# Kernel optimization log

Hardware: AMD Instinct MI355X
Metric: run time of the kernel (lower is better)

Reference implementation:

```python
import jax, jax.numpy as jnp
import numpy as np

HIDDEN = 2048
INTER = 768
NUM_EXPERTS = 32
TOP_K = 4
NUM_TOKENS = 2048


def setup_inputs() -> dict:
    key = jax.random.key(0)
    ks = jax.random.split(key, 5)
    scale = 0.02
    x = jax.random.normal(ks[0], (NUM_TOKENS, HIDDEN), dtype=jnp.float32)
    w_router = jax.random.normal(ks[1], (HIDDEN, NUM_EXPERTS), dtype=jnp.float32) * scale
    w_gate = jax.random.normal(ks[2], (NUM_EXPERTS, HIDDEN, INTER), dtype=jnp.float32) * scale
    w_up = jax.random.normal(ks[3], (NUM_EXPERTS, HIDDEN, INTER), dtype=jnp.float32) * scale
    w_down = jax.random.normal(ks[4], (NUM_EXPERTS, INTER, HIDDEN), dtype=jnp.float32) * scale
    return {"hidden_states": x, "w_router": w_router, "w_gate": w_gate,
            "w_up": w_up, "w_down": w_down}


def reference(hidden_states, w_router, w_gate, w_up, w_down):
    x = hidden_states  # [T, H]
    T = x.shape[0]
    # Router: softmax over experts (in input dtype), top-k, renormalize.
    router_logits = x @ w_router                      # [T, E]
    routing_weights = jax.nn.softmax(router_logits, axis=-1)
    top_w, top_idx = jax.lax.top_k(routing_weights, TOP_K)  # [T, K]
    top_w = top_w / jnp.sum(top_w, axis=-1, keepdims=True)   # norm_topk_prob
    # Dense combine weights: combine[t, e] = routing weight if expert e selected
    # for token t, else 0.  (top-k indices are unique per token.)
    combine = jnp.zeros((T, NUM_EXPERTS), dtype=x.dtype)
    combine = combine.at[jnp.arange(T)[:, None], top_idx].add(top_w)  # [T, E]

    # Scan over experts: each step computes one expert's SwiGLU MLP on all
    # tokens and accumulates it weighted by its combine weight (tokens with
    # zero weight contribute nothing, matching the gather/scatter original).
    def body(acc, expert):
        wg, wu, wd, cw = expert  # [H,I], [H,I], [I,H], [T]
        h = jax.nn.silu(x @ wg) * (x @ wu)   # [T, I]
        return acc + (h @ wd) * cw[:, None], None

    out, _ = jax.lax.scan(body, jnp.zeros_like(x),
                          (w_gate, w_up, w_down, combine.T))
    return out
```

## Files before the change

### kernel.cpp

```cpp
#include <hip/hip_runtime.h>

#define T_TOK 2048
#define HID   2048
#define INTER 768
#define NE    32
#define NSLOT 8192
#define MAXT  96

typedef short bf16x8 __attribute__((ext_vector_type(8)));
typedef float f32x4  __attribute__((ext_vector_type(4)));

#if defined(__has_builtin)
#  if __has_builtin(__builtin_amdgcn_global_load_lds)
#    define HAS_GLDS 1
#  endif
#endif
#ifndef HAS_GLDS
#  define HAS_GLDS 0
#endif

__device__ __forceinline__ unsigned short f2b(float f){
  unsigned u = __builtin_bit_cast(unsigned, f);
  u += 0x7fffu + ((u >> 16) & 1u);
  return (unsigned short)(u >> 16);
}
__device__ __forceinline__ unsigned pk2(float a, float b){
  return (unsigned)f2b(a) | ((unsigned)f2b(b) << 16);
}

__device__ __forceinline__ void stageA16(const ushort* gsrc, ushort* ldst){
#if HAS_GLDS
  __builtin_amdgcn_global_load_lds(
      (const __attribute__((address_space(1))) unsigned int*)gsrc,
      (__attribute__((address_space(3))) unsigned int*)ldst, 16, 0, 0);
#else
  *(uint4*)ldst = *(const uint4*)gsrc;
#endif
}

#define XB_OFF    0ul
#define HBUF_OFF  8388608ul
#define TKW_OFF   20971520ul
#define TKI_OFF   21004288ul
#define ROWS_OFF  21037056ul
#define WTS_OFF   21069824ul
#define OFFS_OFF  21102592ul
#define LOGIT_OFF 21102848ul
#define CNT_OFF   21364992ul
#define FILL_OFF  21365120ul
#define TLIST_OFF 21365248ul
#define T2S_OFF   21365760ul
#define HB2_OFF   21398528ul
#define WS_NEED   (HB2_OFF + 67108864ul)
#define ZERO_OFF  21102848ul
#define ZERO_SZ   (262144ul + 128ul + 128ul)

__global__ void convert_x_kernel(const float* __restrict__ x, ushort* __restrict__ xb){
  int i = (blockIdx.x * 256 + threadIdx.x) * 8;
  float4 a = *(const float4*)(x + i);
  float4 b = *(const float4*)(x + i + 4);
  uint4 o;
  o.x = pk2(a.x, a.y);
  o.y = pk2(a.z, a.w);
  o.z = pk2(b.x, b.y);
  o.w = pk2(b.z, b.w);
  *(uint4*)(xb + i) = o;
}

__global__ void router_gemm(const float* __restrict__ x, const float* __restrict__ wr,
                            float* __restrict__ logits){
  const int tt = blockIdx.x;
  const int kb = blockIdx.y;
  __shared__ float xs[64 * 64];
  __shared__ float wsm[64 * 32];
  const int tid = threadIdx.x;
  const int r = tid >> 5, e = tid & 31;
  float acc[8];
#pragma unroll
  for (int i = 0; i < 8; i++) acc[i] = 0.0f;

  for (int sub = 0; sub < 4; ++sub){
    const int k0 = kb * 256 + sub * 64;
    __syncthreads();
#pragma unroll
    for (int j = 0; j < 4; j++){
      int f4 = tid + j * 256;
      int row = f4 >> 4, c4 = f4 & 15;
      float4 v = *(const float4*)(x + (size_t)(tt * 64 + row) * HID + k0 + c4 * 4);
      *(float4*)(xs + row * 64 + c4 * 4) = v;
    }
#pragma unroll
    for (int j = 0; j < 2; j++){
      int f4 = tid + j * 256;
      int row = f4 >> 3, c4 = f4 & 7;
      float4 v = *(const float4*)(wr + (size_t)(k0 + row) * NE + c4 * 4);
      *(float4*)(wsm + row * NE + c4 * 4) = v;
    }
    __syncthreads();
    for (int kk = 0; kk < 64; kk++){
      float wv = wsm[kk * NE + e];
#pragma unroll
      for (int i = 0; i < 8; i++) acc[i] += xs[(r + i * 8) * 64 + kk] * wv;
    }
  }
#pragma unroll
  for (int i = 0; i < 8; i++)
    atomicAdd(&logits[(size_t)(tt * 64 + r + i * 8) * NE + e], acc[i]);
}

__global__ void topk_kernel(const float* __restrict__ logits, float* __restrict__ topk_w,
                            int* __restrict__ topk_i, int* __restrict__ counts){
  int t = blockIdx.x * blockDim.x + threadIdx.x;
  if (t >= T_TOK) return;
  float l[32];
  const float4* lp = (const float4*)(logits + (size_t)t * NE);
#pragma unroll
  for (int i = 0; i < 8; i++){
    float4 v = lp[i];
    l[i*4+0] = v.x; l[i*4+1] = v.y; l[i*4+2] = v.z; l[i*4+3] = v.w;
  }
  float m = l[0];
#pragma unroll
  for (int i = 1; i < 32; i++) m = fmaxf(m, l[i]);
#pragma unroll
  for (int i = 0; i < 32; i++) l[i] = __expf(l[i] - m);
  float wsel[4]; int isel[4];
#pragma unroll
  for (int k = 0; k < 4; k++){
    float best = l[0]; int bi = 0;
#pragma unroll
    for (int i = 1; i < 32; i++){ if (l[i] > best){ best = l[i]; bi = i; } }
    wsel[k] = best; isel[k] = bi; l[bi] = -1.0f;
  }
  float s4 = wsel[0] + wsel[1] + wsel[2] + wsel[3];
  float inv = 1.0f / s4;
#pragma unroll
  for (int k = 0; k < 4; k++){
    topk_w[t * 4 + k] = wsel[k] * inv;
    topk_i[t * 4 + k] = isel[k];
    atomicAdd(&counts[isel[k]], 1);
  }
}

__global__ void prefix_kernel(const int* __restrict__ counts, int* __restrict__ offsets,
                              int* __restrict__ tlist){
  if (threadIdx.x == 0){
    int a = 0; offsets[0] = 0; int nt_ = 0;
    for (int e = 0; e < NE; e++){
      int c = counts[e];
      for (int m = 0; m * 128 < c && nt_ < MAXT; m++) tlist[nt_++] = e | (m << 16);
      a += c; offsets[e + 1] = a;
    }
    for (; nt_ < MAXT; nt_++) tlist[nt_] = -1;
  }
}

__global__ void scatter_kernel(const int* __restrict__ topk_i, const float* __restrict__ topk_w,
                               const int* __restrict__ offsets, int* __restrict__ fill,
                               int* __restrict__ rows, float* __restrict__ wts,
                               int* __restrict__ t2s){
  int gid = blockIdx.x * 256 + threadIdx.x;
  int t = gid >> 2;
  int e = topk_i[gid];
  int pos = atomicAdd(&fill[e], 1);
  int s = offsets[e] + pos;
  rows[s] = t;
  wts[s] = topk_w[gid];
  t2s[gid] = s;
}

#define NT_GU 64
#define GU_BUF 8192
__global__ __launch_bounds__(512, 6) void gateup_kernel(
    const ushort* __restrict__ xb, const float* __restrict__ wg,
    const float* __restrict__ wu, const int* __restrict__ rows,
    const float* __restrict__ wts, const int* __restrict__ counts,
    const int* __restrict__ offsets, const int* __restrict__ tlist,
    ushort* __restrict__ hbuf)
{
  const int w = tlist[blockIdx.y];
  if (w < 0) return;
  const int e = w & 0xffff, mt = w >> 16;
  const int nt = blockIdx.x;
  const int cnt = counts[e];
  const int off = offsets[e];
  const int n0 = nt * 64;

  __shared__ __align__(16) ushort lds[2 * GU_BUF];

  const int tid = threadIdx.x;

  const int ar = tid >> 2, adc = tid & 3;
  const int alc = adc ^ ((ar >> 1) & 3);
  const int srow = mt * 128 + ar;
  const int tokA = rows[off + (srow < cnt ? srow : 0)];
  const ushort* agp = xb + (size_t)tokA * HID + alc * 8;

  const int bn = tid & 63, kg = tid >> 6;
  const size_t wofs = (size_t)e * (HID * INTER) + (size_t)(kg * 4) * INTER + n0 + bn;
  const float* wgp = wg + wofs;
  const float* wup = wu + wofs;
  const int bofs = bn * 32 + ((kg >> 1) ^ ((bn >> 1) & 3)) * 8 + (kg & 1) * 4;

  const int lane = tid & 63, wv = tid >> 6;
  const int wm = wv >> 1, wn = wv & 1;
  const int fr = lane & 15, ko = lane >> 4;

  int aoff[2], boff[2];
#pragma unroll
  for (int mf = 0; mf < 2; mf++){
    int r = wm * 32 + mf * 16 + fr;
    aoff[mf] = r * 32 + ((ko ^ ((r >> 1) & 3)) * 8);
  }
#pragma unroll
  for (int nf = 0; nf < 2; nf++){
    int c = wn * 32 + nf * 16 + fr;
    boff[nf] = c * 32 + ((ko ^ ((c >> 1) & 3)) * 8);
  }

  f32x4 accg[2][2], accu[2][2];
#pragma unroll
  for (int i = 0; i < 2; i++)
#pragma unroll
    for (int j = 0; j < 2; j++){ accg[i][j] = (f32x4)(0.0f); accu[i][j] = (f32x4)(0.0f); }

  float sg[4], su[4];

  auto loadB = [&](int k0){
    const float* pg_ = wgp + (size_t)k0 * INTER;
    const float* pu_ = wup + (size_t)k0 * INTER;
#pragma unroll
    for (int kk = 0; kk < 4; kk++){ sg[kk] = pg_[(size_t)kk * INTER]; su[kk] = pu_[(size_t)kk * INTER]; }
  };
  auto writeB = [&](int base){
    uint2 pg, pu;
    pg.x = pk2(sg[0], sg[1]); pg.y = pk2(sg[2], sg[3]);
    pu.x = pk2(su[0], su[1]); pu.y = pk2(su[2], su[3]);
    *(uint2*)(lds + base + 4096 + bofs) = pg;
    *(uint2*)(lds + base + 6144 + bofs) = pu;
  };
  auto computeTile = [&](int base){
    bf16x8 a[2], bg2[2], bu2[2];
#pragma unroll
    for (int mf = 0; mf < 2; mf++) a[mf] = *(const bf16x8*)(lds + base + aoff[mf]);
#pragma unroll
    for (int nf = 0; nf < 2; nf++){
      bg2[nf] = *(const bf16x8*)(lds + base + 4096 + boff[nf]);
      bu2[nf] = *(const bf16x8*)(lds + base + 6144 + boff[nf]);
    }
#pragma unroll
    for (int mf = 0; mf < 2; mf++)
#pragma unroll
      for (int nf = 0; nf < 2; nf++){
        accg[mf][nf] = __builtin_amdgcn_mfma_f32_16x16x32_bf16(a[mf], bg2[nf], accg[mf][nf], 0, 0, 0);
        accu[mf][nf] = __builtin_amdgcn_mfma_f32_16x16x32_bf16(a[mf], bu2[nf], accu[mf][nf], 0, 0, 0);
      }
  };

  stageA16(agp, lds + tid * 8);
  loadB(0);
  writeB(0);
  __syncthreads();

  int cb = 0;
  for (int t = 0; t < NT_GU; ++t){
    const int nb = cb ^ GU_BUF;
    if (t + 1 < NT_GU){
      stageA16(agp + (t + 1) * 32, lds + nb + tid * 8);
      loadB((t + 1) * 32);
    }
    computeTile(cb);
    if (t + 1 < NT_GU) writeB(nb);
    __syncthreads();
    cb = nb;
  }

#pragma unroll
  for (int mf = 0; mf < 2; mf++)
#pragma unroll
    for (int j = 0; j < 4; j++){
      int rl = wm * 32 + mf * 16 + ko * 4 + j;
      int gr = mt * 128 + rl;
      if (gr < cnt){
        float w2 = wts[off + gr];
        size_t robase = (size_t)(off + gr) * INTER + n0;
#pragma unroll
        for (int nf = 0; nf < 2; nf++){
          float g = accg[mf][nf][j], u = accu[mf][nf][j];
          float h = (g / (1.0f + __expf(-g))) * u * w2;
          hbuf[robase + wn * 32 + nf * 16 + fr] = f2b(h);
        }
      }
    }
}

#define NT_DN 24
#define DN_BUF 6144
template<bool SLOT>
__global__ __launch_bounds__(512, 6) void down_kernel(
    const ushort* __restrict__ hbuf, const float* __restrict__ wd,
    const int* __restrict__ rows, const int* __restrict__ counts,
    const int* __restrict__ offsets, const int* __restrict__ tlist,
    float* __restrict__ outp)
{
  const int w = tlist[blockIdx.y];
  if (w < 0) return;
  const int e = w & 0xffff, mt = w >> 16;
  const int nt = blockIdx.x;
  const int cnt = counts[e];
  const int off = offsets[e];
  const int n0 = nt * 64;

  __shared__ __align__(16) ushort lds[2 * DN_BUF];

  const int tid = threadIdx.x;

  const int ar = tid >> 2, adc = tid & 3;
  const int alc = adc ^ ((ar >> 1) & 3);
  const int srow = mt * 128 + ar;
  const int slotA = off + (srow < cnt ? srow : 0);
  const ushort* agp = hbuf + (size_t)slotA * INTER + alc * 8;

  const int bn = tid & 63, kg = tid >> 6;
  const float* wdp = wd + (size_t)e * (INTER * HID) + (size_t)(kg * 4) * HID + n0 + bn;
  const int bofs = bn * 32 + ((kg >> 1) ^ ((bn >> 1) & 3)) * 8 + (kg & 1) * 4;

  const int lane = tid & 63, wv = tid >> 6;
  const int wm = wv >> 1, wn = wv & 1;
  const int fr = lane & 15, ko = lane >> 4;

  int aoff[2], boff[2];
#pragma unroll
  for (int mf = 0; mf < 2; mf++){
    int r = wm * 32 + mf * 16 + fr;
    aoff[mf] = r * 32 + ((ko ^ ((r >> 1) & 3)) * 8);
  }
#pragma unroll
  for (int nf = 0; nf < 2; nf++){
    int c = wn * 32 + nf * 16 + fr;
    boff[nf] = c * 32 + ((ko ^ ((c >> 1) & 3)) * 8);
  }

  f32x4 acc[2][2];
#pragma unroll
  for (int i = 0; i < 2; i++)
#pragma unroll
    for (int j = 0; j < 2; j++) acc[i][j] = (f32x4)(0.0f);

  float sb[4];

  auto loadB = [&](int k0){
    const float* p = wdp + (size_t)k0 * HID;
#pragma unroll
    for (int kk = 0; kk < 4; kk++) sb[kk] = p[(size_t)kk * HID];
  };
  auto writeB = [&](int base){
    uint2 pb;
    pb.x = pk2(sb[0], sb[1]); pb.y = pk2(sb[2], sb[3]);
    *(uint2*)(lds + base + 4096 + bofs) = pb;
  };
  auto computeTile = [&](int base){
    bf16x8 a[2], b2[2];
#pragma unroll
    for (int mf = 0; mf < 2; mf++) a[mf] = *(const bf16x8*)(lds + base + aoff[mf]);
#pragma unroll
    for (int nf = 0; nf < 2; nf++) b2[nf] = *(const bf16x8*)(lds + base + 4096 + boff[nf]);
#pragma unroll
    for (int mf = 0; mf < 2; mf++)
#pragma unroll
      for (int nf = 0; nf < 2; nf++)
        acc[mf][nf] = __builtin_amdgcn_mfma_f32_16x16x32_bf16(a[mf], b2[nf], acc[mf][nf], 0, 0, 0);
  };

  stageA16(agp, lds + tid * 8);
  loadB(0);
  writeB(0);
  __syncthreads();

  int cb = 0;
  for (int t = 0; t < NT_DN; ++t){
    const int nb = cb ^ DN_BUF;
    if (t + 1 < NT_DN){
      stageA16(agp + (t + 1) * 32, lds + nb + tid * 8);
      loadB((t + 1) * 32);
    }
    computeTile(cb);
    if (t + 1 < NT_DN) writeB(nb);
    __syncthreads();
    cb = nb;
  }

#pragma unroll
  for (int mf = 0; mf < 2; mf++)
#pragma unroll
    for (int j = 0; j < 4; j++){
      int rl = wm * 32 + mf * 16 + ko * 4 + j;
      int gr = mt * 128 + rl;
      if (gr < cnt){
        if (SLOT){
          float* obase = outp + (size_t)(off + gr) * HID + n0;
#pragma unroll
          for (int nf = 0; nf < 2; nf++)
            obase[wn * 32 + nf * 16 + fr] = acc[mf][nf][j];
        } else {
          int tok = rows[off + gr];
          float* obase = outp + (size_t)tok * HID + n0;
#pragma unroll
          for (int nf = 0; nf < 2; nf++)
            atomicAdd(obase + wn * 32 + nf * 16 + fr, acc[mf][nf][j]);
        }
      }
    }
}

__global__ void combine_kernel(const float* __restrict__ hbuf2, const int* __restrict__ t2s,
                               float* __restrict__ out){
  const int t = blockIdx.y;
  const int c4 = (blockIdx.x * 256 + threadIdx.x) * 4;
  const int s0 = t2s[t * 4 + 0], s1 = t2s[t * 4 + 1];
  const int s2 = t2s[t * 4 + 2], s3 = t2s[t * 4 + 3];
  float4 a = *(const float4*)(hbuf2 + (size_t)s0 * HID + c4);
  float4 b = *(const float4*)(hbuf2 + (size_t)s1 * HID + c4);
  float4 c = *(const float4*)(hbuf2 + (size_t)s2 * HID + c4);
  float4 d = *(const float4*)(hbuf2 + (size_t)s3 * HID + c4);
  float4 r;
  r.x = a.x + b.x + c.x + d.x;
  r.y = a.y + b.y + c.y + d.y;
  r.z = a.z + b.z + c.z + d.z;
  r.w = a.w + b.w + c.w + d.w;
  *(float4*)(out + (size_t)t * HID + c4) = r;
}

extern "C" void kernel_launch(void* const* d_in, const int* in_sizes, int n_in,
                              void* d_out, int out_size, void* d_ws, size_t ws_size,
                              hipStream_t stream){
  const float* x  = (const float*)d_in[0];
  const float* wr = (const float*)d_in[1];
  const float* wg = (const float*)d_in[2];
  const float* wu = (const float*)d_in[3];
  const float* wd = (const float*)d_in[4];
  float* out = (float*)d_out;
  char* ws = (char*)d_ws;

  ushort* xb     = (ushort*)(ws + XB_OFF);
  ushort* hbuf   = (ushort*)(ws + HBUF_OFF);
  float*  topkw  = (float*)(ws + TKW_OFF);
  int*    topki  = (int*)(ws + TKI_OFF);
  int*    rows   = (int*)(ws + ROWS_OFF);
  float*  wts    = (float*)(ws + WTS_OFF);
  int*    offs   = (int*)(ws + OFFS_OFF);
  float*  logits = (float*)(ws + LOGIT_OFF);
  int*    counts = (int*)(ws + CNT_OFF);
  int*    fill   = (int*)(ws + FILL_OFF);
  int*    tlist  = (int*)(ws + TLIST_OFF);
  int*    t2s    = (int*)(ws + T2S_OFF);
  float*  hbuf2  = (float*)(ws + HB2_OFF);

  const bool slotpath = (ws_size >= WS_NEED);

  hipMemsetAsync(ws + ZERO_OFF, 0, ZERO_SZ, stream);

  convert_x_kernel<<<2048, 256, 0, stream>>>(x, xb);
  router_gemm<<<dim3(32, 8), 256, 0, stream>>>(x, wr, logits);
  topk_kernel<<<8, 256, 0, stream>>>(logits, topkw, topki, counts);
  prefix_kernel<<<1, 64, 0, stream>>>(counts, offs, tlist);
  scatter_kernel<<<32, 256, 0, stream>>>(topki, topkw, offs, fill, rows, wts, t2s);
  gateup_kernel<<<dim3(12, MAXT), 512, 0, stream>>>(xb, wg, wu, rows, wts, counts, offs, tlist, hbuf);
  if (slotpath){
    down_kernel<true><<<dim3(32, MAXT), 512, 0, stream>>>(hbuf, wd, rows, counts, offs, tlist, hbuf2);
    combine_kernel<<<dim3(2, T_TOK), 256, 0, stream>>>(hbuf2, t2s, out);
  } else {
    hipMemsetAsync(d_out, 0, (size_t)out_size * sizeof(float), stream);
    down_kernel<false><<<dim3(32, MAXT), 512, 0, stream>>>(hbuf, wd, rows, counts, offs, tlist, out);
  }
}
```

Before: 365.0 us.

## Enlarge MoE GEMM tiles, split gate/up into separate blocks, add SwiGLU fuse kernel

Gate/up and down GEMMs move from 128x64 to 128x256 output tiles, with 16 MFMA accumulators per wave and float4 weight loads in place of scalar strided loads. Gate and up projections now run in separate blocks that write bf16 intermediates. A new elementwise kernel applies SiLU, the multiply and the routing weight. The slot-buffer plus combine path is dropped, so the down projection always accumulates into the output with atomics. The aim is better weight-load coalescing and more operand reuse per tile. The cost is fewer blocks per grid, an extra intermediate round trip, and atomic contention on the output.

```diff
diff --git a/kernel.cpp b/kernel.cpp
--- a/kernel.cpp
+++ b/kernel.cpp
@@ -27,6 +27,10 @@
 __device__ __forceinline__ unsigned pk2(float a, float b){
   return (unsigned)f2b(a) | ((unsigned)f2b(b) << 16);
 }
+__device__ __forceinline__ float b2f(unsigned short u){
+  unsigned x = ((unsigned)u) << 16;
+  return __builtin_bit_cast(float, x);
+}
 
 __device__ __forceinline__ void stageA16(const ushort* gsrc, ushort* ldst){
 #if HAS_GLDS
@@ -39,7 +43,7 @@
 }
 
 #define XB_OFF    0ul
-#define HBUF_OFF  8388608ul
+#define GBUF_OFF  8388608ul
 #define TKW_OFF   20971520ul
 #define TKI_OFF   21004288ul
 #define ROWS_OFF  21037056ul
@@ -49,9 +53,7 @@
 #define CNT_OFF   21364992ul
 #define FILL_OFF  21365120ul
 #define TLIST_OFF 21365248ul
-#define T2S_OFF   21365760ul
-#define HB2_OFF   21398528ul
-#define WS_NEED   (HB2_OFF + 67108864ul)
+#define UBUF_OFF  21365760ul
 #define ZERO_OFF  21102848ul
 #define ZERO_SZ   (262144ul + 128ul + 128ul)
 
@@ -157,8 +159,7 @@
 
 __global__ void scatter_kernel(const int* __restrict__ topk_i, const float* __restrict__ topk_w,
                                const int* __restrict__ offsets, int* __restrict__ fill,
-                               int* __restrict__ rows, float* __restrict__ wts,
-                               int* __restrict__ t2s){
+                               int* __restrict__ rows, float* __restrict__ wts){
   int gid = blockIdx.x * 256 + threadIdx.x;
   int t = gid >> 2;
   int e = topk_i[gid];
@@ -166,95 +167,228 @@
   int s = offsets[e] + pos;
   rows[s] = t;
   wts[s] = topk_w[gid];
-  t2s[gid] = s;
 }
 
 #define NT_GU 64
-#define GU_BUF 8192
-__global__ __launch_bounds__(512, 6) void gateup_kernel(
+#define LDS_STRIDE 12288
+__global__ __launch_bounds__(512) void guv_kernel(
     const ushort* __restrict__ xb, const float* __restrict__ wg,
     const float* __restrict__ wu, const int* __restrict__ rows,
-    const float* __restrict__ wts, const int* __restrict__ counts,
+    const int* __restrict__ counts, const int* __restrict__ offsets,
+    const int* __restrict__ tlist, ushort* __restrict__ gbuf,
+    ushort* __restrict__ ubuf)
+{
+  const int w = tlist[blockIdx.y];
+  if (w < 0) return;
+  const int e = w & 0xffff, mt = w >> 16;
+  const int mat = blockIdx.x & 1, nt = blockIdx.x >> 1;
+  const int cnt = counts[e], off = offsets[e];
+  const int n0 = nt * 256;
+
+  __shared__ __align__(16) ushort lds[2 * LDS_STRIDE + 4096];
+
+  const int tid = threadIdx.x;
+  const int lane = tid & 63, wv = tid >> 6;
+
+  const int ar = tid >> 2;
+  const int aq = (tid & 3) ^ (ar & 3);
+  const int srow = mt * 128 + ar;
+  const int tokA = rows[off + (srow < cnt ? srow : 0)];
+  const ushort* agp = xb + (size_t)tokA * HID + aq * 8;
+
+  const float* wsel = mat ? wu : wg;
+  const float* bgp = wsel + (size_t)e * (HID * INTER) + (size_t)(wv * 4) * INTER + n0 + lane * 4;
+  const int bwbase = lane * 128 + ((wv ^ ((lane & 3) << 1)) << 2);
+
+  const int wm = wv >> 2, wn = wv & 3;
+  const int fr = lane & 15, ko = lane >> 4;
+  int aoff[4], boff[4];
+#pragma unroll
+  for (int mf = 0; mf < 4; mf++){
+    int r = wm * 64 + mf * 16 + fr;
+    aoff[mf] = r * 32 + ((ko ^ (r & 3)) << 3);
+  }
+#pragma unroll
+  for (int nf = 0; nf < 4; nf++){
+    int c = wn * 64 + nf * 16 + fr;
+    boff[nf] = c * 32 + (((ko * 2) ^ (((c >> 2) & 3) << 1)) << 2);
+  }
+
+  f32x4 acc[4][4];
+#pragma unroll
+  for (int i = 0; i < 4; i++)
+#pragma unroll
+    for (int j = 0; j < 4; j++) acc[i][j] = (f32x4)(0.0f);
+
+  float4 br0, br1, br2, br3;
+
+  auto loadB = [&](int k0){
+    br0 = *(const float4*)(bgp + (size_t)(k0 + 0) * INTER);
+    br1 = *(const float4*)(bgp + (size_t)(k0 + 1) * INTER);
+    br2 = *(const float4*)(bgp + (size_t)(k0 + 2) * INTER);
+    br3 = *(const float4*)(bgp + (size_t)(k0 + 3) * INTER);
+  };
+  auto writeB = [&](int cb){
+    ushort* bd = lds + cb + 4096;
+#pragma unroll
+    for (int i = 0; i < 4; i++){
+      uint2 p;
+      p.x = pk2((&br0.x)[i], (&br1.x)[i]);
+      p.y = pk2((&br2.x)[i], (&br3.x)[i]);
+      *(uint2*)(bd + bwbase + i * 32) = p;
+    }
+  };
+  auto compute = [&](int cb){
+    const ushort* A = lds + cb;
+    const ushort* B = lds + cb + 4096;
+    bf16x8 a[4], b[4];
+#pragma unroll
+    for (int mf = 0; mf < 4; mf++) a[mf] = *(const bf16x8*)(A + aoff[mf]);
+#pragma unroll
+    for (int nf = 0; nf < 4; nf++) b[nf] = *(const bf16x8*)(B + boff[nf]);
+#pragma unroll
+    for (int mf = 0; mf < 4; mf++)
+#pragma unroll
+      for (int nf = 0; nf < 4; nf++)
+        acc[mf][nf] = __builtin_amdgcn_mfma_f32_16x16x32_bf16(a[mf], b[nf], acc[mf][nf], 0, 0, 0);
+  };
+
+  stageA16(agp, lds + tid * 8);
+  loadB(0);
+  writeB(0);
+  __syncthreads();
+
+  int cb = 0;
+  for (int t = 0; t < NT_GU; ++t){
+    const int nb = cb ^ LDS_STRIDE;
+    if (t + 1 < NT_GU){
+      stageA16(agp + (t + 1) * 32, lds + nb + tid * 8);
+      loadB((t + 1) * 32);
+    }
+    compute(cb);
+    if (t + 1 < NT_GU) writeB(nb);
+    __syncthreads();
+    cb = nb;
+  }
+
+  ushort* obuf = mat ? ubuf : gbuf;
+#pragma unroll
+  for (int mf = 0; mf < 4; mf++)
+#pragma unroll
+    for (int j = 0; j < 4; j++){
+      int rl = wm * 64 + mf * 16 + ko * 4 + j;
+      int gr = mt * 128 + rl;
+      if (gr < cnt){
+        size_t rb = (size_t)(off + gr) * INTER + n0;
+#pragma unroll
+        for (int nf = 0; nf < 4; nf++)
+          obuf[rb + wn * 64 + nf * 16 + fr] = f2b(acc[mf][nf][j]);
+      }
+    }
+}
+
+__global__ void fuse_kernel(ushort* __restrict__ gbuf, const ushort* __restrict__ ubuf,
+                            const float* __restrict__ wts){
+  const int s = blockIdx.x;
+  const int c = threadIdx.x * 4;
+  const float wt = wts[s];
+  size_t base = (size_t)s * INTER + c;
+  uint2 gv = *(const uint2*)(gbuf + base);
+  uint2 uv = *(const uint2*)(ubuf + base);
+  float h[4];
+  {
+    float g0 = b2f((unsigned short)gv.x),        u0 = b2f((unsigned short)uv.x);
+    float g1 = b2f((unsigned short)(gv.x >> 16)), u1 = b2f((unsigned short)(uv.x >> 16));
+    float g2 = b2f((unsigned short)gv.y),        u2 = b2f((unsigned short)uv.y);
+    float g3 = b2f((unsigned short)(gv.y >> 16)), u3 = b2f((unsigned short)(uv.y >> 16));
+    h[0] = (g0 / (1.0f + __expf(-g0))) * u0 * wt;
+    h[1] = (g1 / (1.0f + __expf(-g1))) * u1 * wt;
+    h[2] = (g2 / (1.0f + __expf(-g2))) * u2 * wt;
+    h[3] = (g3 / (1.0f + __expf(-g3))) * u3 * wt;
+  }
+  uint2 o; o.x = pk2(h[0], h[1]); o.y = pk2(h[2], h[3]);
+  *(uint2*)(gbuf + base) = o;
+}
+
+#define NT_DN 24
+__global__ __launch_bounds__(512) void down_kernel(
+    const ushort* __restrict__ hbuf, const float* __restrict__ wd,
+    const int* __restrict__ rows, const int* __restrict__ counts,
     const int* __restrict__ offsets, const int* __restrict__ tlist,
-    ushort* __restrict__ hbuf)
+    float* __restrict__ out)
 {
   const int w = tlist[blockIdx.y];
   if (w < 0) return;
   const int e = w & 0xffff, mt = w >> 16;
   const int nt = blockIdx.x;
-  const int cnt = counts[e];
-  const int off = offsets[e];
-  const int n0 = nt * 64;
-
-  __shared__ __align__(16) ushort lds[2 * GU_BUF];
+  const int cnt = counts[e], off = offsets[e];
+  const int n0 = nt * 256;
+
+  __shared__ __align__(16) ushort lds[2 * LDS_STRIDE + 4096];
 
   const int tid = threadIdx.x;
-
-  const int ar = tid >> 2, adc = tid & 3;
-  const int alc = adc ^ ((ar >> 1) & 3);
+  const int lane = tid & 63, wv = tid >> 6;
+
+  const int ar = tid >> 2;
+  const int aq = (tid & 3) ^ (ar & 3);
   const int srow = mt * 128 + ar;
-  const int tokA = rows[off + (srow < cnt ? srow : 0)];
-  const ushort* agp = xb + (size_t)tokA * HID + alc * 8;
-
-  const int bn = tid & 63, kg = tid >> 6;
-  const size_t wofs = (size_t)e * (HID * INTER) + (size_t)(kg * 4) * INTER + n0 + bn;
-  const float* wgp = wg + wofs;
-  const float* wup = wu + wofs;
-  const int bofs = bn * 32 + ((kg >> 1) ^ ((bn >> 1) & 3)) * 8 + (kg & 1) * 4;
-
-  const int lane = tid & 63, wv = tid >> 6;
-  const int wm = wv >> 1, wn = wv & 1;
+  const int slotA = off + (srow < cnt ? srow : 0);
+  const ushort* agp = hbuf + (size_t)slotA * INTER + aq * 8;
+
+  const float* bgp = wd + (size_t)e * (INTER * HID) + (size_t)(wv * 4) * HID + n0 + lane * 4;
+  const int bwbase = lane * 128 + ((wv ^ ((lane & 3) << 1)) << 2);
+
+  const int wm = wv >> 2, wn = wv & 3;
   const int fr = lane & 15, ko = lane >> 4;
-
-  int aoff[2], boff[2];
-#pragma unroll
-  for (int mf = 0; mf < 2; mf++){
-    int r = wm * 32 + mf * 16 + fr;
-    aoff[mf] = r * 32 + ((ko ^ ((r >> 1) & 3)) * 8);
-  }
-#pragma unroll
-  for (int nf = 0; nf < 2; nf++){
-    int c = wn * 32 + nf * 16 + fr;
-    boff[nf] = c * 32 + ((ko ^ ((c >> 1) & 3)) * 8);
-  }
-
-  f32x4 accg[2][2], accu[2][2];
-#pragma unroll
-  for (int i = 0; i < 2; i++)
-#pragma unroll
-    for (int j = 0; j < 2; j++){ accg[i][j] = (f32x4)(0.0f); accu[i][j] = (f32x4)(0.0f); }
-
-  float sg[4], su[4];
+  int aoff[4], boff[4];
+#pragma unroll
+  for (int mf = 0; mf < 4; mf++){
+    int r = wm * 64 + mf * 16 + fr;
+    aoff[mf] = r * 32 + ((ko ^ (r & 3)) << 3);
+  }
+#pragma unroll
+  for (int nf = 0; nf < 4; nf++){
+    int c = wn * 64 + nf * 16 + fr;
+    boff[nf] = c * 32 + (((ko * 2) ^ (((c >> 2) & 3) << 1)) << 2);
+  }
+
+  f32x4 acc[4][4];
+#pragma unroll
+  for (int i = 0; i < 4; i++)
+#pragma unroll
+    for (int j = 0; j < 4; j++) acc[i][j] = (f32x4)(0.0f);
+
+  float4 br0, br1, br2, br3;
 
   auto loadB = [&](int k0){
-    const float* pg_ = wgp + (size_t)k0 * INTER;
-    const float* pu_ = wup + (size_t)k0 * INTER;
-#pragma unroll
-    for (int kk = 0; kk < 4; kk++){ sg[kk] = pg_[(size_t)kk * INTER]; su[kk] = pu_[(size_t)kk * INTER]; }
-  };
-  auto writeB = [&](int base){
-    uint2 pg, pu;
-    pg.x = pk2(sg[0], sg[1]); pg.y = pk2(sg[2], sg[3]);
-    pu.x = pk2(su[0], su[1]); pu.y = pk2(su[2], su[3]);
-    *(uint2*)(lds + base + 4096 + bofs) = pg;
-    *(uint2*)(lds + base + 6144 + bofs) = pu;
-  };
-  auto computeTile = [&](int base){
-    bf16x8 a[2], bg2[2], bu2[2];
-#pragma unroll
-    for (int mf = 0; mf < 2; mf++) a[mf] = *(const bf16x8*)(lds + base + aoff[mf]);
-#pragma unroll
-    for (int nf = 0; nf < 2; nf++){
-      bg2[nf] = *(const bf16x8*)(lds + base + 4096 + boff[nf]);
-      bu2[nf] = *(const bf16x8*)(lds + base + 6144 + boff[nf]);
-    }
-#pragma unroll
-    for (int mf = 0; mf < 2; mf++)
-#pragma unroll
-      for (int nf = 0; nf < 2; nf++){
-        accg[mf][nf] = __builtin_amdgcn_mfma_f32_16x16x32_bf16(a[mf], bg2[nf], accg[mf][nf], 0, 0, 0);
-        accu[mf][nf] = __builtin_amdgcn_mfma_f32_16x16x32_bf16(a[mf], bu2[nf], accu[mf][nf], 0, 0, 0);
-      }
+    br0 = *(const float4*)(bgp + (size_t)(k0 + 0) * HID);
+    br1 = *(const float4*)(bgp + (size_t)(k0 + 1) * HID);
+    br2 = *(const float4*)(bgp + (size_t)(k0 + 2) * HID);
+    br3 = *(const float4*)(bgp + (size_t)(k0 + 3) * HID);
+  };
+  auto writeB = [&](int cb){
+    ushort* bd = lds + cb + 4096;
+#pragma unroll
+    for (int i = 0; i < 4; i++){
+      uint2 p;
+      p.x = pk2((&br0.x)[i], (&br1.x)[i]);
+      p.y = pk2((&br2.x)[i], (&br3.x)[i]);
+      *(uint2*)(bd + bwbase + i * 32) = p;
+    }
+  };
+  auto compute = [&](int cb){
+    const ushort* A = lds + cb;
+    const ushort* B = lds + cb + 4096;
+    bf16x8 a[4], b[4];
+#pragma unroll
+    for (int mf = 0; mf < 4; mf++) a[mf] = *(const bf16x8*)(A + aoff[mf]);
+#pragma unroll
+    for (int nf = 0; nf < 4; nf++) b[nf] = *(const bf16x8*)(B + boff[nf]);
+#pragma unroll
+    for (int mf = 0; mf < 4; mf++)
+#pragma unroll
+      for (int nf = 0; nf < 4; nf++)
+        acc[mf][nf] = __builtin_amdgcn_mfma_f32_16x16x32_bf16(a[mf], b[nf], acc[mf][nf], 0, 0, 0);
   };
 
   stageA16(agp, lds + tid * 8);
@@ -263,172 +397,32 @@
   __syncthreads();
 
   int cb = 0;
-  for (int t = 0; t < NT_GU; ++t){
-    const int nb = cb ^ GU_BUF;
-    if (t + 1 < NT_GU){
-      stageA16(agp + (t + 1) * 32, lds + nb + tid * 8);
-      loadB((t + 1) * 32);
-    }
-    computeTile(cb);
-    if (t + 1 < NT_GU) writeB(nb);
-    __syncthreads();
-    cb = nb;
-  }
-
-#pragma unroll
-  for (int mf = 0; mf < 2; mf++)
-#pragma unroll
-    for (int j = 0; j < 4; j++){
-      int rl = wm * 32 + mf * 16 + ko * 4 + j;
-      int gr = mt * 128 + rl;
-      if (gr < cnt){
-        float w2 = wts[off + gr];
-        size_t robase = (size_t)(off + gr) * INTER + n0;
-#pragma unroll
-        for (int nf = 0; nf < 2; nf++){
-          float g = accg[mf][nf][j], u = accu[mf][nf][j];
-          float h = (g / (1.0f + __expf(-g))) * u * w2;
-          hbuf[robase + wn * 32 + nf * 16 + fr] = f2b(h);
-        }
-      }
-    }
-}
-
-#define NT_DN 24
-#define DN_BUF 6144
-template<bool SLOT>
-__global__ __launch_bounds__(512, 6) void down_kernel(
-    const ushort* __restrict__ hbuf, const float* __restrict__ wd,
-    const int* __restrict__ rows, const int* __restrict__ counts,
-    const int* __restrict__ offsets, const int* __restrict__ tlist,
-    float* __restrict__ outp)
-{
-  const int w = tlist[blockIdx.y];
-  if (w < 0) return;
-  const int e = w & 0xffff, mt = w >> 16;
-  const int nt = blockIdx.x;
-  const int cnt = counts[e];
-  const int off = offsets[e];
-  const int n0 = nt * 64;
-
-  __shared__ __align__(16) ushort lds[2 * DN_BUF];
-
-  const int tid = threadIdx.x;
-
-  const int ar = tid >> 2, adc = tid & 3;
-  const int alc = adc ^ ((ar >> 1) & 3);
-  const int srow = mt * 128 + ar;
-  const int slotA = off + (srow < cnt ? srow : 0);
-  const ushort* agp = hbuf + (size_t)slotA * INTER + alc * 8;
-
-  const int bn = tid & 63, kg = tid >> 6;
-  const float* wdp = wd + (size_t)e * (INTER * HID) + (size_t)(kg * 4) * HID + n0 + bn;
-  const int bofs = bn * 32 + ((kg >> 1) ^ ((bn >> 1) & 3)) * 8 + (kg & 1) * 4;
-
-  const int lane = tid & 63, wv = tid >> 6;
-  const int wm = wv >> 1, wn = wv & 1;
-  const int fr = lane & 15, ko = lane >> 4;
-
-  int aoff[2], boff[2];
-#pragma unroll
-  for (int mf = 0; mf < 2; mf++){
-    int r = wm * 32 + mf * 16 + fr;
-    aoff[mf] = r * 32 + ((ko ^ ((r >> 1) & 3)) * 8);
-  }
-#pragma unroll
-  for (int nf = 0; nf < 2; nf++){
-    int c = wn * 32 + nf * 16 + fr;
-    boff[nf] = c * 32 + ((ko ^ ((c >> 1) & 3)) * 8);
-  }
-
-  f32x4 acc[2][2];
-#pragma unroll
-  for (int i = 0; i < 2; i++)
-#pragma unroll
-    for (int j = 0; j < 2; j++) acc[i][j] = (f32x4)(0.0f);
-
-  float sb[4];
-
-  auto loadB = [&](int k0){
-    const float* p = wdp + (size_t)k0 * HID;
-#pragma unroll
-    for (int kk = 0; kk < 4; kk++) sb[kk] = p[(size_t)kk * HID];
-  };
-  auto writeB = [&](int base){
-    uint2 pb;
-    pb.x = pk2(sb[0], sb[1]); pb.y = pk2(sb[2], sb[3]);
-    *(uint2*)(lds + base + 4096 + bofs) = pb;
-  };
-  auto computeTile = [&](int base){
-    bf16x8 a[2], b2[2];
-#pragma unroll
-    for (int mf = 0; mf < 2; mf++) a[mf] = *(const bf16x8*)(lds + base + aoff[mf]);
-#pragma unroll
-    for (int nf = 0; nf < 2; nf++) b2[nf] = *(const bf16x8*)(lds + base + 4096 + boff[nf]);
-#pragma unroll
-    for (int mf = 0; mf < 2; mf++)
-#pragma unroll
-      for (int nf = 0; nf < 2; nf++)
-        acc[mf][nf] = __builtin_amdgcn_mfma_f32_16x16x32_bf16(a[mf], b2[nf], acc[mf][nf], 0, 0, 0);
-  };
-
-  stageA16(agp, lds + tid * 8);
-  loadB(0);
-  writeB(0);
-  __syncthreads();
-
-  int cb = 0;
   for (int t = 0; t < NT_DN; ++t){
-    const int nb = cb ^ DN_BUF;
+    const int nb = cb ^ LDS_STRIDE;
     if (t + 1 < NT_DN){
       stageA16(agp + (t + 1) * 32, lds + nb + tid * 8);
       loadB((t + 1) * 32);
     }
-    computeTile(cb);
+    compute(cb);
     if (t + 1 < NT_DN) writeB(nb);
     __syncthreads();
     cb = nb;
   }
 
 #pragma unroll
-  for (int mf = 0; mf < 2; mf++)
+  for (int mf = 0; mf < 4; mf++)
 #pragma unroll
     for (int j = 0; j < 4; j++){
-      int rl = wm * 32 + mf * 16 + ko * 4 + j;
+      int rl = wm * 64 + mf * 16 + ko * 4 + j;
       int gr = mt * 128 + rl;
       if (gr < cnt){
-        if (SLOT){
-          float* obase = outp + (size_t)(off + gr) * HID + n0;
-#pragma unroll
-          for (int nf = 0; nf < 2; nf++)
-            obase[wn * 32 + nf * 16 + fr] = acc[mf][nf][j];
-        } else {
-          int tok = rows[off + gr];
-          float* obase = outp + (size_t)tok * HID + n0;
-#pragma unroll
-          for (int nf = 0; nf < 2; nf++)
-            atomicAdd(obase + wn * 32 + nf * 16 + fr, acc[mf][nf][j]);
-        }
+        int tok = rows[off + gr];
+        float* obase = out + (size_t)tok * HID + n0;
+#pragma unroll
+        for (int nf = 0; nf < 4; nf++)
+          atomicAdd(obase + wn * 64 + nf * 16 + fr, acc[mf][nf][j]);
       }
     }
-}
-
-__global__ void combine_kernel(const float* __restrict__ hbuf2, const int* __restrict__ t2s,
-                               float* __restrict__ out){
-  const int t = blockIdx.y;
-  const int c4 = (blockIdx.x * 256 + threadIdx.x) * 4;
-  const int s0 = t2s[t * 4 + 0], s1 = t2s[t * 4 + 1];
-  const int s2 = t2s[t * 4 + 2], s3 = t2s[t * 4 + 3];
-  float4 a = *(const float4*)(hbuf2 + (size_t)s0 * HID + c4);
-  float4 b = *(const float4*)(hbuf2 + (size_t)s1 * HID + c4);
-  float4 c = *(const float4*)(hbuf2 + (size_t)s2 * HID + c4);
-  float4 d = *(const float4*)(hbuf2 + (size_t)s3 * HID + c4);
-  float4 r;
-  r.x = a.x + b.x + c.x + d.x;
-  r.y = a.y + b.y + c.y + d.y;
-  r.z = a.z + b.z + c.z + d.z;
-  r.w = a.w + b.w + c.w + d.w;
-  *(float4*)(out + (size_t)t * HID + c4) = r;
 }
 
 extern "C" void kernel_launch(void* const* d_in, const int* in_sizes, int n_in,
@@ -443,7 +437,8 @@
   char* ws = (char*)d_ws;
 
   ushort* xb     = (ushort*)(ws + XB_OFF);
-  ushort* hbuf   = (ushort*)(ws + HBUF_OFF);
+  ushort* gbuf   = (ushort*)(ws + GBUF_OFF);
+  ushort* ubuf   = (ushort*)(ws + UBUF_OFF);
   float*  topkw  = (float*)(ws + TKW_OFF);
   int*    topki  = (int*)(ws + TKI_OFF);
   int*    rows   = (int*)(ws + ROWS_OFF);
@@ -453,24 +448,16 @@
   int*    counts = (int*)(ws + CNT_OFF);
   int*    fill   = (int*)(ws + FILL_OFF);
   int*    tlist  = (int*)(ws + TLIST_OFF);
-  int*    t2s    = (int*)(ws + T2S_OFF);
-  float*  hbuf2  = (float*)(ws + HB2_OFF);
-
-  const bool slotpath = (ws_size >= WS_NEED);
 
   hipMemsetAsync(ws + ZERO_OFF, 0, ZERO_SZ, stream);
+  hipMemsetAsync(d_out, 0, (size_t)out_size * sizeof(float), stream);
 
   convert_x_kernel<<<2048, 256, 0, stream>>>(x, xb);
   router_gemm<<<dim3(32, 8), 256, 0, stream>>>(x, wr, logits);
   topk_kernel<<<8, 256, 0, stream>>>(logits, topkw, topki, counts);
   prefix_kernel<<<1, 64, 0, stream>>>(counts, offs, tlist);
-  scatter_kernel<<<32, 256, 0, stream>>>(topki, topkw, offs, fill, rows, wts, t2s);
-  gateup_kernel<<<dim3(12, MAXT), 512, 0, stream>>>(xb, wg, wu, rows, wts, counts, offs, tlist, hbuf);
-  if (slotpath){
-    down_kernel<true><<<dim3(32, MAXT), 512, 0, stream>>>(hbuf, wd, rows, counts, offs, tlist, hbuf2);
-    combine_kernel<<<dim3(2, T_TOK), 256, 0, stream>>>(hbuf2, t2s, out);
-  } else {
-    hipMemsetAsync(d_out, 0, (size_t)out_size * sizeof(float), stream);
-    down_kernel<false><<<dim3(32, MAXT), 512, 0, stream>>>(hbuf, wd, rows, counts, offs, tlist, out);
-  }
-}
+  scatter_kernel<<<32, 256, 0, stream>>>(topki, topkw, offs, fill, rows, wts);
+  guv_kernel<<<dim3(6, MAXT), 512, 0, stream>>>(xb, wg, wu, rows, counts, offs, tlist, gbuf, ubuf);
+  fuse_kernel<<<NSLOT, 192, 0, stream>>>(gbuf, ubuf, wts);
+  down_kernel<<<dim3(8, MAXT), 512, 0, stream>>>(gbuf, wd, rows, counts, offs, tlist, out);
+}
```

Result: faster. 356.3 us (-2.4%).
